# Kernel tuning notes

Hardware: AMD Instinct MI355X
Metric: run time of the kernel (lower is better)

## Reference

```python
import jax, jax.numpy as jnp
from jax import lax
import numpy as np

BN_EPS = 1e-5


def conv_transpose2d(x, w, b, stride, pad):
    # torch ConvTranspose2d weight layout: (in, out, kH, kW)
    k = w.shape[2]
    wt = jnp.flip(w, (2, 3)).transpose(1, 0, 2, 3)  # (out, in, kH, kW)
    p = k - 1 - pad
    out = lax.conv_general_dilated(
        x, wt, window_strides=(1, 1), padding=[(p, p), (p, p)],
        lhs_dilation=(stride, stride),
        dimension_numbers=("NCHW", "OIHW", "NCHW"))
    return out + b[None, :, None, None]


def conv2d(x, w, b, pad):
    out = lax.conv_general_dilated(
        x, w, window_strides=(1, 1), padding=[(pad, pad), (pad, pad)],
        dimension_numbers=("NCHW", "OIHW", "NCHW"))
    return out + b[None, :, None, None]


def batchnorm2d(x, gamma, beta):
    # training-mode BN: batch statistics over (N, H, W), biased variance
    mean = jnp.mean(x, axis=(0, 2, 3), keepdims=True)
    var = jnp.mean((x - mean) ** 2, axis=(0, 2, 3), keepdims=True)
    xn = (x - mean) * lax.rsqrt(var + BN_EPS)
    return xn * gamma[None, :, None, None] + beta[None, :, None, None]


def setup_inputs():
    key = jax.random.key(0)
    ks = jax.random.split(key, 8)
    B = 4096
    return {
        "x": jax.random.randint(ks[0], (B,), 0, 60032, dtype=jnp.int32),
        "encoder_w": jax.random.normal(ks[1], (60032, 7 * 7 * 64), jnp.float32) * 0.02,
        "emb_w": jax.random.normal(ks[2], (512, 64), jnp.float32) * 0.02,
        "deconv1_w": jax.random.normal(ks[3], (64, 32, 4, 4), jnp.float32) * 0.03,
        "deconv1_b": jnp.zeros((32,), jnp.float32),
        "bn1_g": jnp.ones((32,), jnp.float32),
        "bn1_b": jnp.zeros((32,), jnp.float32),
        "deconv2_w": jax.random.normal(ks[4], (32, 16, 4, 4), jnp.float32) * 0.04,
        "deconv2_b": jnp.zeros((16,), jnp.float32),
        "bn2_g": jnp.ones((16,), jnp.float32),
        "bn2_b": jnp.zeros((16,), jnp.float32),
        "conv_w": jax.random.normal(ks[5], (1, 16, 3, 3), jnp.float32) * 0.08,
        "conv_b": jnp.zeros((1,), jnp.float32),
    }


def reference(x, encoder_w, emb_w, deconv1_w, deconv1_b, bn1_g, bn1_b,
              deconv2_w, deconv2_b, bn2_g, bn2_b, conv_w, conv_b):
    # encoder embedding lookup -> [B, 64, 7, 7]
    z_e_x = encoder_w[x].reshape(-1, 64, 7, 7)
    z = z_e_x.transpose(0, 2, 3, 1)  # [B, H, W, C]
    # squared L2 distances to codebook, computed without the [B,H,W,C,K] blowup:
    # ||z||^2 - 2 z.e + ||e||^2, identical math to the broadcast-pow-sum
    d = ((z ** 2).sum(-1, keepdims=True)
         - 2.0 * jnp.einsum("bhwc,kc->bhwk", z, emb_w)
         + (emb_w ** 2).sum(-1))  # [B, H, W, K]
    latents = jnp.argmin(d, axis=-1)  # [B, H, W]
    z_q_x = emb_w[latents].transpose(0, 3, 1, 2)  # [B, 64, 7, 7]
    # decoder
    h = jax.nn.relu(batchnorm2d(conv_transpose2d(z_q_x, deconv1_w, deconv1_b, 2, 1), bn1_g, bn1_b))
    h = jax.nn.relu(batchnorm2d(conv_transpose2d(h, deconv2_w, deconv2_b, 2, 1), bn2_g, bn2_b))
    x_tilde = jax.nn.sigmoid(conv2d(h, conv_w, conv_b, 1))  # [B, 1, 28, 28]
    return (x_tilde, z_e_x, z_q_x)
```

## Files before the change

kernel.cpp:

```cpp
#include <hip/hip_runtime.h>
#include <hip/hip_bf16.h>
#include <math.h>

#define BATCH   4096
#define CH      64
#define KCB     512

#define XT_N    (BATCH*784)
#define ZE_OFF  (XT_N)
#define ZQ_OFF  (XT_N + BATCH*3136)

#define WS_C1   0
#define WS_C2   102760448ULL
#define WS_ST   308281344ULL
#define WS_BN   308282112ULL
#define WS_WF2  308282496ULL
#define WS_EF   308298880ULL
#define WS_EE   308429952ULL
#define WS_WF1  WS_C2

typedef __attribute__((ext_vector_type(8))) __bf16 bf16x8;
typedef __attribute__((ext_vector_type(4))) float f32x4;
union B8 { uint4 u; bf16x8 v; };

__device__ inline unsigned short f2bf(float f) {
    unsigned int u = __float_as_uint(f);
    u = u + 0x7fffu + ((u >> 16) & 1u);
    return (unsigned short)(u >> 16);
}
__device__ inline float bf2f(unsigned short h) {
    return __uint_as_float(((unsigned int)h) << 16);
}

__global__ void k_zero(double* __restrict__ stats) {
    int t = threadIdx.x;
    if (t < 96) stats[t] = 0.0;
}

__global__ void k_prep(const float* __restrict__ w1, const float* __restrict__ w2,
                       const float* __restrict__ emb,
                       unsigned short* __restrict__ w1f, unsigned short* __restrict__ w2f,
                       unsigned short* __restrict__ ef, float* __restrict__ eeW) {
    int t = threadIdx.x + blockIdx.x * 256;
    {
        int i = t & 7, lane = (t >> 3) & 63, frag = t >> 9;
        int mt = frag >> 2, khalf = (frag >> 1) & 1, hilo = frag & 1;
        int cw = mt * 16 + (lane & 15);
        int k  = khalf * 32 + ((lane >> 4) << 3) + i;
        float v = emb[(cw << 6) + k];
        unsigned short h = f2bf(v);
        ef[t] = hilo ? f2bf(v - bf2f(h)) : h;
    }
    if (t < 32768) {
        int i = t & 7, lane = (t >> 3) & 63, frag = t >> 9;
        int cls = frag >> 4, tap = (frag >> 2) & 3, khalf = (frag >> 1) & 1, mt = frag & 1;
        int ph = cls >> 1, pw = cls & 1, dh = tap >> 1, dw = tap & 1;
        int kh = (1 - ph) + 2 * dh, kw = (1 - pw) + 2 * dw;
        int oc = mt * 16 + (lane & 15);
        int ic = khalf * 32 + ((lane >> 4) << 3) + i;
        w1f[t] = f2bf(w1[((ic * 32 + oc) << 4) + kh * 4 + kw]);
    }
    if (t < 8192) {
        int i = t & 7, lane = (t >> 3) & 63, frag = t >> 9;
        int cls = frag >> 2, tap = frag & 3;
        int ph = cls >> 1, pw = cls & 1, dh = tap >> 1, dw = tap & 1;
        int kh = (1 - ph) + 2 * dh, kw = (1 - pw) + 2 * dw;
        int oc = lane & 15;
        int ic = ((lane >> 4) << 3) + i;
        w2f[t] = f2bf(w2[((ic * 16 + oc) << 4) + kh * 4 + kw]);
    }
    if (t < KCB) {
        double s = 0.0;
        const float* e = emb + (t << 6);
        for (int c = 0; c < CH; ++c) s += (double)e[c] * (double)e[c];
        eeW[t] = (float)s;
    }
}

__global__ __launch_bounds__(256) void k1_encode(
    const int* __restrict__ xidx, const float* __restrict__ encW,
    const float* __restrict__ emb, const unsigned short* __restrict__ ef,
    const float* __restrict__ eeW, float* __restrict__ out)
{
    __shared__ __align__(16) unsigned short zh_s[128*72];
    __shared__ __align__(16) unsigned short zl_s[128*72];
    __shared__ float ee_s[KCB];
    __shared__ float zzp[128][2];

    const int tid = threadIdx.x, wave = tid >> 6, lane = tid & 63;
    const int blk = blockIdx.x;

    for (int k = tid; k < KCB; k += 256) ee_s[k] = eeW[k];

    {
        const int pos = tid & 127, h = tid >> 7;
        float zacc = 0.f;
        const int p  = blk*128 + pos;
        const int b  = p / 49;
        const int hw = p - b*49;
        const long long row = xidx[b];
        const float* rp = encW + row*3136LL + hw;
        float* zep = out + ZE_OFF + (long long)b*3136 + hw;
        #pragma unroll
        for (int j = 0; j < 32; ++j) {
            int c = h + 2*j;
            float v = rp[c*49];
            zep[c*49] = v;
            unsigned short hb = f2bf(v);
            float r = v - bf2f(hb);
            zh_s[pos*72 + c] = hb;
            zl_s[pos*72 + c] = f2bf(r);
            zacc = fmaf(v, v, zacc);
        }
        zzp[pos][h] = zacc;
    }
    __syncthreads();

    const int col = lane & 15, g = lane >> 4;
    B8 Bh[2][2], Bl[2][2];
    #pragma unroll
    for (int t2 = 0; t2 < 2; ++t2) {
        int pos = (wave*2 + t2)*16 + col;
        #pragma unroll
        for (int kh = 0; kh < 2; ++kh) {
            Bh[t2][kh].u = *(const uint4*)(zh_s + pos*72 + kh*32 + g*8);
            Bl[t2][kh].u = *(const uint4*)(zl_s + pos*72 + kh*32 + g*8);
        }
    }

    float d0[2] = {3.4e38f, 3.4e38f}, d1[2] = {3.4e38f, 3.4e38f};
    int   k0[2] = {0, 0},             k1i[2] = {1, 1};

    const uint4* ap = (const uint4*)ef + lane;
    uint4 A0 = ap[0*64], A1 = ap[1*64], A2 = ap[2*64], A3 = ap[3*64];

    for (int mt = 0; mt < 32; ++mt) {
        B8 Ah0, Al0, Ah1, Al1;
        Ah0.u = A0; Al0.u = A1; Ah1.u = A2; Al1.u = A3;
        if (mt < 31) {
            const uint4* np = ap + (mt+1)*256;
            A0 = np[0]; A1 = np[64]; A2 = np[128]; A3 = np[192];
        }
        const float4 eev = *(const float4*)&ee_s[mt*16 + (g << 2)];
        #pragma unroll
        for (int t2 = 0; t2 < 2; ++t2) {
            f32x4 acc = {eev.x*-0.5f, eev.y*-0.5f, eev.z*-0.5f, eev.w*-0.5f};
            acc = __builtin_amdgcn_mfma_f32_16x16x32_bf16(Ah0.v, Bh[t2][0].v, acc, 0,0,0);
            acc = __builtin_amdgcn_mfma_f32_16x16x32_bf16(Ah1.v, Bh[t2][1].v, acc, 0,0,0);
            acc = __builtin_amdgcn_mfma_f32_16x16x32_bf16(Ah0.v, Bl[t2][0].v, acc, 0,0,0);
            acc = __builtin_amdgcn_mfma_f32_16x16x32_bf16(Ah1.v, Bl[t2][1].v, acc, 0,0,0);
            acc = __builtin_amdgcn_mfma_f32_16x16x32_bf16(Al0.v, Bh[t2][0].v, acc, 0,0,0);
            acc = __builtin_amdgcn_mfma_f32_16x16x32_bf16(Al1.v, Bh[t2][1].v, acc, 0,0,0);
            #pragma unroll
            for (int rg = 0; rg < 4; ++rg) {
                float s = -2.f * acc[rg];
                int  cw = mt*16 + (g << 2) + rg;
                if (s < d0[t2] || (s == d0[t2] && cw < k0[t2])) {
                    d1[t2] = d0[t2]; k1i[t2] = k0[t2]; d0[t2] = s; k0[t2] = cw;
                } else if (s < d1[t2] || (s == d1[t2] && cw < k1i[t2])) {
                    d1[t2] = s; k1i[t2] = cw;
                }
            }
        }
    }

    #pragma unroll
    for (int t2 = 0; t2 < 2; ++t2) {
        #pragma unroll
        for (int msk = 16; msk <= 32; msk <<= 1) {
            float e0 = __shfl_xor(d0[t2], msk), e1 = __shfl_xor(d1[t2], msk);
            int   j0 = __shfl_xor(k0[t2], msk), j1 = __shfl_xor(k1i[t2], msk);
            if (e0 < d0[t2] || (e0 == d0[t2] && j0 < k0[t2])) {
                if (d0[t2] < e1 || (d0[t2] == e1 && k0[t2] < j1)) { d1[t2] = d0[t2]; k1i[t2] = k0[t2]; }
                else                                              { d1[t2] = e1;     k1i[t2] = j1;     }
                d0[t2] = e0; k0[t2] = j0;
            } else {
                if (e0 < d1[t2] || (e0 == d1[t2] && j0 < k1i[t2])) { d1[t2] = e0; k1i[t2] = j0; }
            }
        }

        const int pos = (wave*2 + t2)*16 + col;
        const int p   = blk*128 + pos;
        const int b   = p / 49;
        const int hw  = p - b*49;
        const float zz = zzp[pos][0] + zzp[pos][1];
        int win = k0[t2];

        if (d1[t2] - d0[t2] < fmaxf(1e-6f, 1e-3f * fabsf(d0[t2] + zz))) {
            const float* zp = out + ZE_OFF + (long long)b*3136 + hw;
            const float* ea = emb + k0[t2]*CH;
            const float* eb = emb + k1i[t2]*CH;
            double D0 = 0.0, D1 = 0.0;
            for (int c = 0; c < CH; ++c) {
                double zv = (double)zp[c*49];
                double f0 = zv - (double)ea[c];
                double f1 = zv - (double)eb[c];
                D0 += f0*f0; D1 += f1*f1;
            }
            if (D1 < D0 || (D1 == D0 && k1i[t2] < k0[t2])) win = k1i[t2];
        }

        float* zqp = out + ZQ_OFF + (long long)b*3136 + hw;
        const float* e0p = emb + win*CH + g*16;
        #pragma unroll
        for (int j = 0; j < 16; ++j) zqp[(g*16 + j)*49] = e0p[j];
    }
}

__global__ __launch_bounds__(256) void k2_deconv1(
    const float* __restrict__ zq, const unsigned short* __restrict__ w1f,
    const float* __restrict__ b1, float* __restrict__ c1cls,
    double* __restrict__ stats)
{
    __shared__ __align__(16) unsigned short x_s[2*81*72];
    __shared__ float bs[32], bq[32];

    const int tid = threadIdx.x, wave = tid >> 6, lane = tid & 63;
    const int b0 = blockIdx.x << 1;

    for (int i = tid; i < 2*81*72/2; i += 256) ((unsigned int*)x_s)[i] = 0u;
    if (tid < 32) { bs[tid] = 0.f; bq[tid] = 0.f; }
    __syncthreads();

    for (int i = tid; i < 6272; i += 256) {
        int img = i >= 3136;
        int e = i - img*3136;
        int c = e / 49, hw = e - c*49;
        int ih = hw / 7, iw = hw - ih*7;
        float v = zq[(long long)(b0+img)*3136 + e];
        x_s[img*5832 + ((ih+1)*9 + (iw+1))*72 + c] = f2bf(v);
    }
    __syncthreads();

    const int cls = wave, ph = cls >> 1, pw = cls & 1;
    bf16x8 wfr[4][2][2];
    {
        const uint4* wp = (const uint4*)w1f + (cls*16)*64 + lane;
        #pragma unroll
        for (int tap = 0; tap < 4; ++tap)
            #pragma unroll
            for (int kh2 = 0; kh2 < 2; ++kh2)
                #pragma unroll
                for (int mt = 0; mt < 2; ++mt) {
                    B8 t; t.u = wp[(tap*4 + kh2*2 + mt)*64];
                    wfr[tap][kh2][mt] = t.v;
                }
    }
    float biasv[2][4];
    #pragma unroll
    for (int mt = 0; mt < 2; ++mt)
        #pragma unroll
        for (int rg = 0; rg < 4; ++rg)
            biasv[mt][rg] = b1[mt*16 + ((lane >> 4) << 2) + rg];

    float ts[2][4] = {{0.f}}, tq[2][4] = {{0.f}};
    const int gb = (lane >> 4) << 4;

    for (int nt = 0; nt < 7; ++nt) {
        int m = nt*16 + (lane & 15);
        bool valid = m < 98;
        int mm = valid ? m : 0;
        int img = mm >= 49;
        int px = mm - img*49;
        int a = px / 7, bb = px - a*7;
        f32x4 acc0 = {0.f,0.f,0.f,0.f}, acc1 = {0.f,0.f,0.f,0.f};
        #pragma unroll
        for (int dh = 0; dh < 2; ++dh)
            #pragma unroll
            for (int dw = 0; dw < 2; ++dw) {
                int tap = dh*2 + dw;
                int r = (a + ph - dh + 1)*9 + (bb + pw - dw + 1);
                const char* p = (const char*)x_s + img*11664 + r*144 + gb;
                B8 x0; x0.u = *(const uint4*)p;
                B8 x1; x1.u = *(const uint4*)(p + 64);
                acc0 = __builtin_amdgcn_mfma_f32_16x16x32_bf16(wfr[tap][0][0], x0.v, acc0, 0,0,0);
                acc1 = __builtin_amdgcn_mfma_f32_16x16x32_bf16(wfr[tap][0][1], x0.v, acc1, 0,0,0);
                acc0 = __builtin_amdgcn_mfma_f32_16x16x32_bf16(wfr[tap][1][0], x1.v, acc0, 0,0,0);
                acc1 = __builtin_amdgcn_mfma_f32_16x16x32_bf16(wfr[tap][1][1], x1.v, acc1, 0,0,0);
            }
        if (valid) {
            float* base = c1cls + (long long)(b0+img)*6272 + cls*1568 + px;
            #pragma unroll
            for (int rg = 0; rg < 4; ++rg) {
                int oc = ((lane >> 4) << 2) + rg;
                float v0 = acc0[rg] + biasv[0][rg];
                float v1 = acc1[rg] + biasv[1][rg];
                base[oc*49]      = v0;
                base[(oc+16)*49] = v1;
                ts[0][rg] += v0; tq[0][rg] = fmaf(v0, v0, tq[0][rg]);
                ts[1][rg] += v1; tq[1][rg] = fmaf(v1, v1, tq[1][rg]);
            }
        }
    }

    #pragma unroll
    for (int mt = 0; mt < 2; ++mt)
        #pragma unroll
        for (int rg = 0; rg < 4; ++rg) {
            float s = ts[mt][rg], q = tq[mt][rg];
            #pragma unroll
            for (int msk = 1; msk < 16; msk <<= 1) {
                s += __shfl_xor(s, msk);
                q += __shfl_xor(q, msk);
            }
            if ((lane & 15) == 0) {
                int oc = mt*16 + ((lane >> 4) << 2) + rg;
                atomicAdd(&bs[oc], s);
                atomicAdd(&bq[oc], q);
            }
        }
    __syncthreads();
    if (tid < 32) {
        atomicAdd(&stats[tid],      (double)bs[tid]);
        atomicAdd(&stats[32 + tid], (double)bq[tid]);
    }
}

__global__ void k_bnfin(const double* __restrict__ stats, const float* __restrict__ g,
                        const float* __restrict__ be, float* __restrict__ bn,
                        int soff, int boff, int nch, double n)
{
    int t = threadIdx.x;
    if (t < nch) {
        double mean = stats[soff + t] / n;
        double var  = stats[soff + nch + t] / n - mean*mean;
        double rstd = 1.0 / sqrt(var + 1e-5);
        double sc   = (double)g[t] * rstd;
        bn[boff + t]       = (float)sc;
        bn[boff + nch + t] = (float)((double)be[t] - mean*sc);
    }
}

__global__ __launch_bounds__(256) void k4_deconv2(
    const float* __restrict__ c1cls, const unsigned short* __restrict__ w2f,
    const float* __restrict__ b2, const float* __restrict__ bn,
    float* __restrict__ c2cls, double* __restrict__ stats)
{
    __shared__ __align__(16) unsigned short x_s[256*40];
    __shared__ float bnl[64];
    __shared__ float bs[16], bq[16];

    const int tid = threadIdx.x, wave = tid >> 6, lane = tid & 63;
    const int b = blockIdx.x;

    for (int i = tid; i < 256*40/2; i += 256) ((unsigned int*)x_s)[i] = 0u;
    if (tid < 64) bnl[tid] = bn[tid];
    if (tid < 16) { bs[tid] = 0.f; bq[tid] = 0.f; }
    __syncthreads();

    const float* cb = c1cls + (long long)b*6272;
    for (int i = tid; i < 6272; i += 256) {
        int cl = i / 1568, e = i - cl*1568;
        int ic = e / 49, pxc = e - ic*49;
        int a = pxc / 7, bb = pxc - a*7;
        int ih = 2*a + (cl >> 1), iw = 2*bb + (cl & 1);
        float v = fmaxf(fmaf(cb[i], bnl[ic], bnl[32 + ic]), 0.f);
        x_s[((ih+1)*16 + (iw+1))*40 + ic] = f2bf(v);
    }
    __syncthreads();

    const int cls = wave, ph = cls >> 1, pw = cls & 1;
    bf16x8 wfr[4];
    {
        const uint4* wp = (const uint4*)w2f + (cls*4)*64 + lane;
        #pragma unroll
        for (int tap = 0; tap < 4; ++tap) { B8 t; t.u = wp[tap*64]; wfr[tap] = t.v; }
    }
    float biasv[4];
    #pragma unroll
    for (int rg = 0; rg < 4; ++rg) biasv[rg] = b2[((lane >> 4) << 2) + rg];

    float ts[4] = {0.f}, tq[4] = {0.f};
    float* c2b = c2cls + (long long)b*12544 + cls*3136;
    const int gb = (lane >> 4) << 4;

    for (int nt = 0; nt < 13; ++nt) {
        int m = nt*16 + (lane & 15);
        bool valid = m < 196;
        int px = valid ? m : 0;
        int a = px / 14, bb = px - a*14;
        f32x4 acc = {0.f,0.f,0.f,0.f};
        #pragma unroll
        for (int dh = 0; dh < 2; ++dh)
            #pragma unroll
            for (int dw = 0; dw < 2; ++dw) {
                int tap = dh*2 + dw;
                int r = (a + ph - dh + 1)*16 + (bb + pw - dw + 1);
                B8 x0; x0.u = *(const uint4*)((const char*)x_s + r*80 + gb);
                acc = __builtin_amdgcn_mfma_f32_16x16x32_bf16(wfr[tap], x0.v, acc, 0,0,0);
            }
        if (valid) {
            float* base = c2b + px;
            #pragma unroll
            for (int rg = 0; rg < 4; ++rg) {
                int oc = ((lane >> 4) << 2) + rg;
                float v = acc[rg] + biasv[rg];
                base[oc*196] = v;
                ts[rg] += v; tq[rg] = fmaf(v, v, tq[rg]);
            }
        }
    }

    #pragma unroll
    for (int rg = 0; rg < 4; ++rg) {
        float s = ts[rg], q = tq[rg];
        #pragma unroll
        for (int msk = 1; msk < 16; msk <<= 1) {
            s += __shfl_xor(s, msk);
            q += __shfl_xor(q, msk);
        }
        if ((lane & 15) == 0) {
            int oc = ((lane >> 4) << 2) + rg;
            atomicAdd(&bs[oc], s);
            atomicAdd(&bq[oc], q);
        }
    }
    __syncthreads();
    if (tid < 16) {
        atomicAdd(&stats[64 + tid], (double)bs[tid]);
        atomicAdd(&stats[80 + tid], (double)bq[tid]);
    }
}

__global__ __launch_bounds__(256) void k6_conv(
    const float* __restrict__ c2cls, const float* __restrict__ cw,
    const float* __restrict__ cbias, const float* __restrict__ bn,
    float* __restrict__ out)
{
    __shared__ float x_s[9*31*16];
    __shared__ float w_s[144];

    const int tid  = threadIdx.x;
    const int b    = blockIdx.x >> 2;
    const int qrt  = blockIdx.x & 3;
    const int r0   = qrt*7 - 1;

    for (int i = tid; i < 9*31*16; i += 256) x_s[i] = 0.f;
    if (tid < 144) {
        int ic = tid / 9, khw = tid - ic*9;
        w_s[khw*16 + ic] = cw[tid];
    }
    __syncthreads();

    const float* cr = c2cls + (long long)b*12544;
    for (int i = tid; i < 4032; i += 256) {
        int c = i / 252, rem = i - c*252;
        int rr = rem / 28, iw = rem - rr*28;
        int ih = r0 + rr;
        if ((unsigned)ih < 28u) {
            int cl  = ((ih & 1) << 1) | (iw & 1);
            int px2 = (ih >> 1)*14 + (iw >> 1);
            float v = fmaxf(fmaf(cr[cl*3136 + c*196 + px2], bn[64 + c], bn[80 + c]), 0.f);
            x_s[(rr*31 + (iw+1))*16 + c] = v;
        }
    }
    __syncthreads();

    const float bias = cbias[0];
    const int px = tid;
    if (px < 196) {
        int ohl = px / 28, ow = px - ohl*28;
        float a0=0.f,a1=0.f,a2=0.f,a3=0.f;
        #pragma unroll
        for (int kh = 0; kh < 3; ++kh) {
            #pragma unroll
            for (int kw = 0; kw < 3; ++kw) {
                const float4* xv = (const float4*)&x_s[((ohl+kh)*31 + ow+kw)*16];
                const float4* wv = (const float4*)&w_s[((kh*3 + kw) << 4)];
                #pragma unroll
                for (int c4 = 0; c4 < 4; ++c4) {
                    float4 xx = xv[c4];
                    float4 ww = wv[c4];
                    a0 = fmaf(xx.x, ww.x, a0);
                    a1 = fmaf(xx.y, ww.y, a1);
                    a2 = fmaf(xx.z, ww.z, a2);
                    a3 = fmaf(xx.w, ww.w, a3);
                }
            }
        }
        float t = ((a0+a1) + (a2+a3)) + bias;
        out[(long long)b*784 + (qrt*7 + ohl)*28 + ow] = 1.f / (1.f + expf(-t));
    }
}

extern "C" void kernel_launch(void* const* d_in, const int* in_sizes, int n_in,
                              void* d_out, int out_size, void* d_ws, size_t ws_size,
                              hipStream_t stream) {
    const int*   x    = (const int*)d_in[0];
    const float* encW = (const float*)d_in[1];
    const float* emb  = (const float*)d_in[2];
    const float* w1   = (const float*)d_in[3];
    const float* b1   = (const float*)d_in[4];
    const float* g1   = (const float*)d_in[5];
    const float* be1  = (const float*)d_in[6];
    const float* w2   = (const float*)d_in[7];
    const float* b2   = (const float*)d_in[8];
    const float* g2   = (const float*)d_in[9];
    const float* be2  = (const float*)d_in[10];
    const float* cw   = (const float*)d_in[11];
    const float* cb   = (const float*)d_in[12];
    float* out = (float*)d_out;

    char* ws = (char*)d_ws;
    float*          c1cls = (float*)(ws + WS_C1);
    float*          c2cls = (float*)(ws + WS_C2);
    double*         stats = (double*)(ws + WS_ST);
    float*          bnbuf = (float*)(ws + WS_BN);
    unsigned short* w1f   = (unsigned short*)(ws + WS_WF1);
    unsigned short* w2f   = (unsigned short*)(ws + WS_WF2);
    unsigned short* ef    = (unsigned short*)(ws + WS_EF);
    float*          eeW   = (float*)(ws + WS_EE);

    k_zero<<<1, 128, 0, stream>>>(stats);
    k_prep<<<256, 256, 0, stream>>>(w1, w2, emb, w1f, w2f, ef, eeW);
    k1_encode<<<1568, 256, 0, stream>>>(x, encW, emb, ef, eeW, out);
    k2_deconv1<<<2048, 256, 0, stream>>>(out + ZQ_OFF, w1f, b1, c1cls, stats);
    k_bnfin<<<1, 64, 0, stream>>>(stats, g1, be1, bnbuf, 0, 0, 32, 4096.0*196.0);
    k4_deconv2<<<4096, 256, 0, stream>>>(c1cls, w2f, b2, bnbuf, c2cls, stats);
    k_bnfin<<<1, 64, 0, stream>>>(stats, g2, be2, bnbuf, 64, 64, 16, 4096.0*784.0);
    k6_conv<<<16384, 256, 0, stream>>>(c2cls, cw, cb, bnbuf, out);
}
```

Baseline: 496.4 us.

## Store deconv intermediates in bf16 and fold BN finalize into consumer kernels

Deconv1 and deconv2 outputs are now written to the workspace as bf16 instead of fp32, which halves the traffic for the two large intermediate tensors. The BN statistics finalize is computed inside the consuming kernels (deconv2 and the final conv), and stats zeroing moves into k_prep, removing three tiny kernel launches. This costs bf16 rounding of the pre-BN activations and redundant per-block finalize math.

```diff
diff --git a/kernel.cpp b/kernel.cpp
--- a/kernel.cpp
+++ b/kernel.cpp
@@ -11,12 +11,11 @@
 #define ZQ_OFF  (XT_N + BATCH*3136)
 
 #define WS_C1   0
-#define WS_C2   102760448ULL
-#define WS_ST   308281344ULL
-#define WS_BN   308282112ULL
-#define WS_WF2  308282496ULL
-#define WS_EF   308298880ULL
-#define WS_EE   308429952ULL
+#define WS_C2   51380224ULL
+#define WS_ST   154140672ULL
+#define WS_WF2  154141824ULL
+#define WS_EF   154158208ULL
+#define WS_EE   154289280ULL
 #define WS_WF1  WS_C2
 
 typedef __attribute__((ext_vector_type(8))) __bf16 bf16x8;
@@ -32,16 +31,13 @@
     return __uint_as_float(((unsigned int)h) << 16);
 }
 
-__global__ void k_zero(double* __restrict__ stats) {
-    int t = threadIdx.x;
-    if (t < 96) stats[t] = 0.0;
-}
-
 __global__ void k_prep(const float* __restrict__ w1, const float* __restrict__ w2,
                        const float* __restrict__ emb,
                        unsigned short* __restrict__ w1f, unsigned short* __restrict__ w2f,
-                       unsigned short* __restrict__ ef, float* __restrict__ eeW) {
+                       unsigned short* __restrict__ ef, float* __restrict__ eeW,
+                       double* __restrict__ stats) {
     int t = threadIdx.x + blockIdx.x * 256;
+    if (t < 96) stats[t] = 0.0;
     {
         int i = t & 7, lane = (t >> 3) & 63, frag = t >> 9;
         int mt = frag >> 2, khalf = (frag >> 1) & 1, hilo = frag & 1;
@@ -209,7 +205,7 @@
 
 __global__ __launch_bounds__(256) void k2_deconv1(
     const float* __restrict__ zq, const unsigned short* __restrict__ w1f,
-    const float* __restrict__ b1, float* __restrict__ c1cls,
+    const float* __restrict__ b1, unsigned short* __restrict__ c1cls,
     double* __restrict__ stats)
 {
     __shared__ __align__(16) unsigned short x_s[2*81*72];
@@ -279,14 +275,14 @@
                 acc1 = __builtin_amdgcn_mfma_f32_16x16x32_bf16(wfr[tap][1][1], x1.v, acc1, 0,0,0);
             }
         if (valid) {
-            float* base = c1cls + (long long)(b0+img)*6272 + cls*1568 + px;
+            unsigned short* base = c1cls + (long long)(b0+img)*6272 + cls*1568 + px;
             #pragma unroll
             for (int rg = 0; rg < 4; ++rg) {
                 int oc = ((lane >> 4) << 2) + rg;
                 float v0 = acc0[rg] + biasv[0][rg];
                 float v1 = acc1[rg] + biasv[1][rg];
-                base[oc*49]      = v0;
-                base[(oc+16)*49] = v1;
+                base[oc*49]      = f2bf(v0);
+                base[(oc+16)*49] = f2bf(v1);
                 ts[0][rg] += v0; tq[0][rg] = fmaf(v0, v0, tq[0][rg]);
                 ts[1][rg] += v1; tq[1][rg] = fmaf(v1, v1, tq[1][rg]);
             }
@@ -316,25 +312,11 @@
     }
 }
 
-__global__ void k_bnfin(const double* __restrict__ stats, const float* __restrict__ g,
-                        const float* __restrict__ be, float* __restrict__ bn,
-                        int soff, int boff, int nch, double n)
-{
-    int t = threadIdx.x;
-    if (t < nch) {
-        double mean = stats[soff + t] / n;
-        double var  = stats[soff + nch + t] / n - mean*mean;
-        double rstd = 1.0 / sqrt(var + 1e-5);
-        double sc   = (double)g[t] * rstd;
-        bn[boff + t]       = (float)sc;
-        bn[boff + nch + t] = (float)((double)be[t] - mean*sc);
-    }
-}
-
 __global__ __launch_bounds__(256) void k4_deconv2(
-    const float* __restrict__ c1cls, const unsigned short* __restrict__ w2f,
-    const float* __restrict__ b2, const float* __restrict__ bn,
-    float* __restrict__ c2cls, double* __restrict__ stats)
+    const unsigned short* __restrict__ c1cls, const unsigned short* __restrict__ w2f,
+    const float* __restrict__ b2, const float* __restrict__ g1,
+    const float* __restrict__ be1, double* stats,
+    unsigned short* __restrict__ c2cls)
 {
     __shared__ __align__(16) unsigned short x_s[256*40];
     __shared__ float bnl[64];
@@ -344,17 +326,25 @@
     const int b = blockIdx.x;
 
     for (int i = tid; i < 256*40/2; i += 256) ((unsigned int*)x_s)[i] = 0u;
-    if (tid < 64) bnl[tid] = bn[tid];
+    if (tid < 32) {
+        const double n = 4096.0*196.0;
+        double mean = stats[tid] / n;
+        double var  = stats[32 + tid] / n - mean*mean;
+        double rstd = 1.0 / sqrt(var + 1e-5);
+        double sc   = (double)g1[tid] * rstd;
+        bnl[tid]      = (float)sc;
+        bnl[32 + tid] = (float)((double)be1[tid] - mean*sc);
+    }
     if (tid < 16) { bs[tid] = 0.f; bq[tid] = 0.f; }
     __syncthreads();
 
-    const float* cb = c1cls + (long long)b*6272;
+    const unsigned short* cb = c1cls + (long long)b*6272;
     for (int i = tid; i < 6272; i += 256) {
         int cl = i / 1568, e = i - cl*1568;
         int ic = e / 49, pxc = e - ic*49;
         int a = pxc / 7, bb = pxc - a*7;
         int ih = 2*a + (cl >> 1), iw = 2*bb + (cl & 1);
-        float v = fmaxf(fmaf(cb[i], bnl[ic], bnl[32 + ic]), 0.f);
+        float v = fmaxf(fmaf(bf2f(cb[i]), bnl[ic], bnl[32 + ic]), 0.f);
         x_s[((ih+1)*16 + (iw+1))*40 + ic] = f2bf(v);
     }
     __syncthreads();
@@ -371,7 +361,7 @@
     for (int rg = 0; rg < 4; ++rg) biasv[rg] = b2[((lane >> 4) << 2) + rg];
 
     float ts[4] = {0.f}, tq[4] = {0.f};
-    float* c2b = c2cls + (long long)b*12544 + cls*3136;
+    unsigned short* c2b = c2cls + (long long)b*12544 + cls*3136;
     const int gb = (lane >> 4) << 4;
 
     for (int nt = 0; nt < 13; ++nt) {
@@ -390,12 +380,12 @@
                 acc = __builtin_amdgcn_mfma_f32_16x16x32_bf16(wfr[tap], x0.v, acc, 0,0,0);
             }
         if (valid) {
-            float* base = c2b + px;
+            unsigned short* base = c2b + px;
             #pragma unroll
             for (int rg = 0; rg < 4; ++rg) {
                 int oc = ((lane >> 4) << 2) + rg;
                 float v = acc[rg] + biasv[rg];
-                base[oc*196] = v;
+                base[oc*196] = f2bf(v);
                 ts[rg] += v; tq[rg] = fmaf(v, v, tq[rg]);
             }
         }
@@ -423,12 +413,14 @@
 }
 
 __global__ __launch_bounds__(256) void k6_conv(
-    const float* __restrict__ c2cls, const float* __restrict__ cw,
-    const float* __restrict__ cbias, const float* __restrict__ bn,
+    const unsigned short* __restrict__ c2cls, const float* __restrict__ cw,
+    const float* __restrict__ cbias, const float* __restrict__ g2,
+    const float* __restrict__ be2, const double* __restrict__ stats,
     float* __restrict__ out)
 {
     __shared__ float x_s[9*31*16];
     __shared__ float w_s[144];
+    __shared__ float bn2[32];
 
     const int tid  = threadIdx.x;
     const int b    = blockIdx.x >> 2;
@@ -440,9 +432,19 @@
         int ic = tid / 9, khw = tid - ic*9;
         w_s[khw*16 + ic] = cw[tid];
     }
-    __syncthreads();
-
-    const float* cr = c2cls + (long long)b*12544;
+    if (tid >= 192 && tid < 208) {
+        int c = tid - 192;
+        const double n = 4096.0*784.0;
+        double mean = stats[64 + c] / n;
+        double var  = stats[80 + c] / n - mean*mean;
+        double rstd = 1.0 / sqrt(var + 1e-5);
+        double sc   = (double)g2[c] * rstd;
+        bn2[c]      = (float)sc;
+        bn2[16 + c] = (float)((double)be2[c] - mean*sc);
+    }
+    __syncthreads();
+
+    const unsigned short* cr = c2cls + (long long)b*12544;
     for (int i = tid; i < 4032; i += 256) {
         int c = i / 252, rem = i - c*252;
         int rr = rem / 28, iw = rem - rr*28;
@@ -450,7 +452,7 @@
         if ((unsigned)ih < 28u) {
             int cl  = ((ih & 1) << 1) | (iw & 1);
             int px2 = (ih >> 1)*14 + (iw >> 1);
-            float v = fmaxf(fmaf(cr[cl*3136 + c*196 + px2], bn[64 + c], bn[80 + c]), 0.f);
+            float v = fmaxf(fmaf(bf2f(cr[cl*3136 + c*196 + px2]), bn2[c], bn2[16 + c]), 0.f);
             x_s[(rr*31 + (iw+1))*16 + c] = v;
         }
     }
@@ -502,21 +504,17 @@
     float* out = (float*)d_out;
 
     char* ws = (char*)d_ws;
-    float*          c1cls = (float*)(ws + WS_C1);
-    float*          c2cls = (float*)(ws + WS_C2);
+    unsigned short* c1cls = (unsigned short*)(ws + WS_C1);
+    unsigned short* c2cls = (unsigned short*)(ws + WS_C2);
     double*         stats = (double*)(ws + WS_ST);
-    float*          bnbuf = (float*)(ws + WS_BN);
     unsigned short* w1f   = (unsigned short*)(ws + WS_WF1);
     unsigned short* w2f   = (unsigned short*)(ws + WS_WF2);
     unsigned short* ef    = (unsigned short*)(ws + WS_EF);
     float*          eeW   = (float*)(ws + WS_EE);
 
-    k_zero<<<1, 128, 0, stream>>>(stats);
-    k_prep<<<256, 256, 0, stream>>>(w1, w2, emb, w1f, w2f, ef, eeW);
+    k_prep<<<256, 256, 0, stream>>>(w1, w2, emb, w1f, w2f, ef, eeW, stats);
     k1_encode<<<1568, 256, 0, stream>>>(x, encW, emb, ef, eeW, out);
     k2_deconv1<<<2048, 256, 0, stream>>>(out + ZQ_OFF, w1f, b1, c1cls, stats);
-    k_bnfin<<<1, 64, 0, stream>>>(stats, g1, be1, bnbuf, 0, 0, 32, 4096.0*196.0);
-    k4_deconv2<<<4096, 256, 0, stream>>>(c1cls, w2f, b2, bnbuf, c2cls, stats);
-    k_bnfin<<<1, 64, 0, stream>>>(stats, g2, be2, bnbuf, 64, 64, 16, 4096.0*784.0);
-    k6_conv<<<16384, 256, 0, stream>>>(c2cls, cw, cb, bnbuf, out);
-}
+    k4_deconv2<<<4096, 256, 0, stream>>>(c1cls, w2f, b2, g1, be1, stats, c2cls);
+    k6_conv<<<16384, 256, 0, stream>>>(c2cls, cw, cb, g2, be2, stats, out);
+}
```

After: 465.3 us. -6.3%, faster.
